# Kernel tuning notes

Hardware: AMD Instinct MI355X
Metric: run time of the kernel (lower is better)

## Reference

```python
import jax, jax.numpy as jnp
import numpy as np

NEG_BIG = -1e38

def setup_inputs() -> dict:
    key = jax.random.key(0)
    kq, kk, kv, kwq, kwk = jax.random.split(key, 5)
    B, S, d_model, d_k, d_v = 4, 4096, 256, 64, 64
    return {
        "q": jax.random.normal(kq, (B, S, d_model), dtype=jnp.float32),
        "k": jax.random.normal(kk, (B, S, d_model), dtype=jnp.float32),
        "v": jax.random.normal(kv, (B, S, d_v), dtype=jnp.float32),
        "w_q": jax.random.normal(kwq, (d_k, d_model), dtype=jnp.float32) * 0.01,
        "w_k": jax.random.normal(kwk, (d_k, d_model), dtype=jnp.float32) * 0.01,
    }

def reference(q, k, v, w_q, w_k):
    d_k = w_q.shape[0]
    temperature = jnp.asarray(np.power(d_k, 0.5), dtype=q.dtype)
    # relu-projected Q, K: [B,S,d_k]
    qp = jax.nn.relu(jnp.einsum("bsm,km->bsk", q, w_q))
    kp = jax.nn.relu(jnp.einsum("bsm,km->bsk", k, w_k))
    # scores [B,S,S]
    attn = jnp.einsum("bqd,bkd->bqk", qp, kp) / temperature
    # force column 0 to -1e38 (inline custom mask)
    attn = attn.at[:, :, 0].set(NEG_BIG)
    attn = jax.nn.softmax(attn, axis=2)
    # dropout is identity in eval / p=0
    out = jnp.einsum("bqk,bkd->bqd", attn, v)
    return out
```

## Files before the change

### kernel.cpp

```cpp
#include <hip/hip_runtime.h>

#define B_    4
#define S_    4096
#define DM    256
#define DK    64
#define NROWS (B_ * S_)
#define LOG2E 1.4426950408889634f
#define PACK_BIAS 0.0028151295f

typedef __attribute__((ext_vector_type(8))) short bfrag;
typedef __attribute__((ext_vector_type(4))) float ffrag;

__device__ __forceinline__ unsigned bf16_rne_hi(float x) {
    unsigned u = __float_as_uint(x);
    return u + 0x7fffu + ((u >> 16) & 1u);
}
__device__ __forceinline__ unsigned short f2bf(float x) {
    return (unsigned short)(bf16_rne_hi(x) >> 16);
}
__device__ __forceinline__ unsigned pack_bf16x2(float lo, float hi) {
    return (bf16_rne_hi(hi) & 0xffff0000u) | (bf16_rne_hi(lo) >> 16);
}

__device__ __forceinline__ float fast_exp2(float x) {
#if __has_builtin(__builtin_amdgcn_exp2f)
    return __builtin_amdgcn_exp2f(x);
#else
    float r;
    asm("v_exp_f32 %0, %1\n\ts_nop 1" : "=v"(r) : "v"(x));
    return r;
#endif
}

__device__ __forceinline__ unsigned trunc_pack_bf16x2(float lo, float hi) {
    return __builtin_amdgcn_perm(__float_as_uint(hi), __float_as_uint(lo),
                                 0x07060302u);
}

__device__ __forceinline__ void proj_step(
    const float4 xv0, const float4 xv1, const unsigned short* wlds,
    int kf, int m, int quad, ffrag acc[4])
{
    union { bfrag v; unsigned u[4]; } pk;
    pk.u[0] = pack_bf16x2(xv0.x, xv0.y);
    pk.u[1] = pack_bf16x2(xv0.z, xv0.w);
    pk.u[2] = pack_bf16x2(xv1.x, xv1.y);
    pk.u[3] = pack_bf16x2(xv1.z, xv1.w);
#pragma unroll
    for (int dt = 0; dt < 4; ++dt) {
        const bfrag Bf = *(const bfrag*)&wlds[(dt * 16 + m) * 264 + kf * 32 + quad * 8];
        acc[dt] = __builtin_amdgcn_mfma_f32_16x16x32_bf16(pk.v, Bf, acc[dt], 0, 0, 0);
    }
}

__global__ __launch_bounds__(256) void fused_prep(
    const float* __restrict__ q, const float* __restrict__ k,
    const float* __restrict__ v, const float* __restrict__ wq,
    const float* __restrict__ wk, unsigned short* __restrict__ vT,
    unsigned short* __restrict__ qpb, unsigned short* __restrict__ kpb)
{
    __shared__ __align__(16) char smem[64 * 264 * 2];
    const int blk  = blockIdx.x;
    const int tid  = threadIdx.x;
    const int lane = tid & 63, w = tid >> 6;

    if (blk < 256) {
        float (*tile)[65] = (float(*)[65])smem;
        const int b = blk >> 6, s0 = (blk & 63) * 64;
#pragma unroll
        for (int i = 0; i < 16; ++i) {
            const int sl = i * 4 + w;
            tile[sl][lane] = v[(b * S_ + s0 + sl) * DK + lane];
        }
        __syncthreads();
        const int t32 = lane >> 5, pos = lane & 31;
        const int keyl = t32 * 32 + ((pos & 1) ? (pos >> 1) + 16 : (pos >> 1));
#pragma unroll
        for (int i = 0; i < 16; ++i) {
            const int d = i * 4 + w;
            vT[((size_t)(b * 128 + (s0 >> 5) + t32) * 64 + d) * 32 + pos] =
                f2bf(tile[keyl][d]);
        }
    } else {
        unsigned short* wlds = (unsigned short*)smem;
        const int pb = blk - 256;
        const int half = pb >> 8, rblk = pb & 255;
        const float* x;
        const float* wsrc;
        unsigned short* o;
        float scale;
        if (half == 0) { x = q; wsrc = wq; o = qpb; scale = 0.125f * LOG2E; }
        else           { x = k; wsrc = wk; o = kpb; scale = 1.0f; }

        const int m = lane & 15, quad = lane >> 4;
        const int rows0 = rblk * 64 + w * 16;
        const float* xrow = x + (size_t)(rows0 + m) * DM + quad * 8;
        const float4* xf4 = (const float4*)xrow;

        float4 xA[4][2];
#pragma unroll
        for (int t = 0; t < 4; ++t) {
            xA[t][0] = xf4[t * 8];
            xA[t][1] = xf4[t * 8 + 1];
        }

#pragma unroll
        for (int i = 0; i < 16; ++i) {
            const int idx4 = i * 256 + tid;
            const int r = idx4 >> 6, c4 = idx4 & 63;
            const float4 wv = ((const float4*)wsrc)[idx4];
            uint2 pk;
            pk.x = pack_bf16x2(wv.x, wv.y);
            pk.y = pack_bf16x2(wv.z, wv.w);
            *(uint2*)&wlds[r * 264 + c4 * 4] = pk;
        }
        __syncthreads();

        ffrag acc[4];
#pragma unroll
        for (int dt = 0; dt < 4; ++dt) acc[dt] = (ffrag)(0.0f);

        float4 xB[4][2];
#pragma unroll
        for (int kf = 0; kf < 4; ++kf) {
            xB[kf][0] = xf4[(kf + 4) * 8];
            xB[kf][1] = xf4[(kf + 4) * 8 + 1];
            proj_step(xA[kf][0], xA[kf][1], wlds, kf, m, quad, acc);
        }
#pragma unroll
        for (int kf = 0; kf < 4; ++kf)
            proj_step(xB[kf][0], xB[kf][1], wlds, kf + 4, m, quad, acc);

#pragma unroll
        for (int dt = 0; dt < 4; ++dt)
#pragma unroll
            for (int r = 0; r < 4; ++r)
                o[(rows0 + quad * 4 + r) * DK + dt * 16 + m] =
                    f2bf(fmaxf(acc[dt][r], 0.0f) * scale);
    }
}

__global__ __launch_bounds__(256) void attn_mfma(
    const unsigned short* __restrict__ qp, const unsigned short* __restrict__ kp,
    const unsigned short* __restrict__ vT, float* __restrict__ out)
{
    __shared__ __align__(16) char smem[20480];
    unsigned short* Plds = (unsigned short*)smem;
    float* red0 = (float*)smem;
    float* red1 = (float*)smem + 2560;

    const int lane = threadIdx.x & 63, w = threadIdx.x >> 6;
    const int m = lane & 15, quad = lane >> 4;

    const int flat = blockIdx.x;
    const int qg   = ((flat & 7) << 6) | (flat >> 3);

    const int qbase = qg * 32;
    const int b = qg >> 7;
    const int kstart = w * 1024;

    bfrag qa[2][2];
#pragma unroll
    for (int mt = 0; mt < 2; ++mt)
#pragma unroll
        for (int kf = 0; kf < 2; ++kf)
            qa[mt][kf] = *(const bfrag*)&qp[(qbase + mt * 16 + m) * DK + kf * 32 + quad * 8];

    ffrag oacc[2][4];
    float dacc[2][4];
#pragma unroll
    for (int mt = 0; mt < 2; ++mt) {
#pragma unroll
        for (int dt = 0; dt < 4; ++dt) oacc[mt][dt] = (ffrag)(0.0f);
#pragma unroll
        for (int r = 0; r < 4; ++r) dacc[mt][r] = 0.0f;
    }

    const unsigned short* kptr = kp + ((size_t)b * S_ + kstart + m) * DK + quad * 8;
    const unsigned short* vptr = vT + ((size_t)(b * 128 + (kstart >> 5)) * 64 + m) * 32 + quad * 8;
    unsigned short* Pw = Plds + w * 1280;

    const ffrag cbias = (ffrag)(PACK_BIAS);

    bfrag kbuf[2][2][2], vbuf[2][4];
#pragma unroll
    for (int kt = 0; kt < 2; ++kt)
#pragma unroll
        for (int kf = 0; kf < 2; ++kf)
            kbuf[0][kt][kf] = *(const bfrag*)(kptr + kt * 1024 + kf * 32);
#pragma unroll
    for (int dt = 0; dt < 4; ++dt)
        vbuf[0][dt] = *(const bfrag*)(vptr + dt * 512);

    bfrag pa0, pa1;

#pragma unroll 2
    for (int jj = 0; jj < 32; ++jj) {
        const int p = jj & 1;

        if (jj < 31) {
            const unsigned short* kn = kptr + (jj + 1) * 2048;
#pragma unroll
            for (int kt = 0; kt < 2; ++kt)
#pragma unroll
                for (int kf = 0; kf < 2; ++kf)
                    kbuf[p ^ 1][kt][kf] = *(const bfrag*)(kn + kt * 1024 + kf * 32);
        }

        if (jj > 0) {
#pragma unroll
            for (int dt = 0; dt < 4; ++dt) {
                oacc[0][dt] = __builtin_amdgcn_mfma_f32_16x16x32_bf16(pa0, vbuf[p ^ 1][dt], oacc[0][dt], 0, 0, 0);
                oacc[1][dt] = __builtin_amdgcn_mfma_f32_16x16x32_bf16(pa1, vbuf[p ^ 1][dt], oacc[1][dt], 0, 0, 0);
            }
        }

        if (jj < 31) {
            const unsigned short* vn = vptr + (jj + 1) * 2048;
#pragma unroll
            for (int dt = 0; dt < 4; ++dt)
                vbuf[p ^ 1][dt] = *(const bfrag*)(vn + dt * 512);
        }

        ffrag s[2][2];
#pragma unroll
        for (int mt = 0; mt < 2; ++mt)
#pragma unroll
            for (int kt = 0; kt < 2; ++kt) {
                ffrag t = __builtin_amdgcn_mfma_f32_16x16x32_bf16(qa[mt][0], kbuf[p][kt][0], cbias, 0, 0, 0);
                s[mt][kt] = __builtin_amdgcn_mfma_f32_16x16x32_bf16(qa[mt][1], kbuf[p][kt][1], t, 0, 0, 0);
            }

        const bool mask0 = (jj == 0) && (w == 0) && (m == 0);
#pragma unroll
        for (int mt = 0; mt < 2; ++mt)
#pragma unroll
            for (int r = 0; r < 4; ++r) {
                float e0 = fast_exp2(s[mt][0][r]);
                float e1 = fast_exp2(s[mt][1][r]);
                if (mask0) e0 = 0.0f;
                dacc[mt][r] += e0 + e1;
                *(unsigned*)&Pw[(mt * 16 + quad * 4 + r) * 40 + m * 2] =
                    trunc_pack_bf16x2(e0, e1);
            }

        pa0 = *(const bfrag*)&Pw[(m) * 40 + quad * 8];
        pa1 = *(const bfrag*)&Pw[(16 + m) * 40 + quad * 8];
    }
#pragma unroll
    for (int dt = 0; dt < 4; ++dt) {
        oacc[0][dt] = __builtin_amdgcn_mfma_f32_16x16x32_bf16(pa0, vbuf[1][dt], oacc[0][dt], 0, 0, 0);
        oacc[1][dt] = __builtin_amdgcn_mfma_f32_16x16x32_bf16(pa1, vbuf[1][dt], oacc[1][dt], 0, 0, 0);
    }

#pragma unroll
    for (int mt = 0; mt < 2; ++mt)
#pragma unroll
        for (int r = 0; r < 4; ++r) {
            float d = dacc[mt][r];
            d += __shfl_xor(d, 1, 64);
            d += __shfl_xor(d, 2, 64);
            d += __shfl_xor(d, 4, 64);
            d += __shfl_xor(d, 8, 64);
            dacc[mt][r] = d;
        }

    __syncthreads();
    if (w >= 2) {
        float* dst = (w == 2) ? red0 : red1;
#pragma unroll
        for (int mt = 0; mt < 2; ++mt) {
#pragma unroll
            for (int dt = 0; dt < 4; ++dt)
#pragma unroll
                for (int r = 0; r < 4; ++r)
                    dst[((mt * 4 + dt) * 4 + r) * 64 + lane] = oacc[mt][dt][r];
#pragma unroll
            for (int r = 0; r < 4; ++r)
                dst[2048 + (mt * 4 + r) * 64 + lane] = dacc[mt][r];
        }
    }
    __syncthreads();
    if (w < 2) {
        const float* src = (w == 0) ? red0 : red1;
#pragma unroll
        for (int mt = 0; mt < 2; ++mt) {
#pragma unroll
            for (int dt = 0; dt < 4; ++dt)
#pragma unroll
                for (int r = 0; r < 4; ++r)
                    oacc[mt][dt][r] += src[((mt * 4 + dt) * 4 + r) * 64 + lane];
#pragma unroll
            for (int r = 0; r < 4; ++r)
                dacc[mt][r] += src[2048 + (mt * 4 + r) * 64 + lane];
        }
    }
    __syncthreads();
    if (w == 1) {
#pragma unroll
        for (int mt = 0; mt < 2; ++mt) {
#pragma unroll
            for (int dt = 0; dt < 4; ++dt)
#pragma unroll
                for (int r = 0; r < 4; ++r)
                    red0[((mt * 4 + dt) * 4 + r) * 64 + lane] = oacc[mt][dt][r];
#pragma unroll
            for (int r = 0; r < 4; ++r)
                red0[2048 + (mt * 4 + r) * 64 + lane] = dacc[mt][r];
        }
    }
    __syncthreads();
    if (w == 0) {
#pragma unroll
        for (int mt = 0; mt < 2; ++mt) {
            float invd[4];
#pragma unroll
            for (int r = 0; r < 4; ++r) {
                const float dv = dacc[mt][r] + red0[2048 + (mt * 4 + r) * 64 + lane];
                invd[r] = 1.0f / dv;
            }
#pragma unroll
            for (int dt = 0; dt < 4; ++dt)
#pragma unroll
                for (int r = 0; r < 4; ++r) {
                    const float nv = oacc[mt][dt][r] + red0[((mt * 4 + dt) * 4 + r) * 64 + lane];
                    out[(size_t)(qbase + mt * 16 + quad * 4 + r) * DK + dt * 16 + m] =
                        nv * invd[r];
                }
        }
    }
}

extern "C" void kernel_launch(void* const* d_in, const int* in_sizes, int n_in,
                              void* d_out, int out_size, void* d_ws, size_t ws_size,
                              hipStream_t stream)
{
    const float* q  = (const float*)d_in[0];
    const float* k  = (const float*)d_in[1];
    const float* v  = (const float*)d_in[2];
    const float* wq = (const float*)d_in[3];
    const float* wk = (const float*)d_in[4];
    float* out = (float*)d_out;

    char* p = (char*)d_ws;
    unsigned short* qpb = (unsigned short*)p;   p += (size_t)NROWS * DK * 2;
    unsigned short* kpb = (unsigned short*)p;   p += (size_t)NROWS * DK * 2;
    unsigned short* vT  = (unsigned short*)p;

    fused_prep<<<768, 256, 0, stream>>>(q, k, v, wq, wk, vT, qpb, kpb);
    attn_mfma<<<512, 256, 0, stream>>>(qpb, kpb, vT, out);
}
```

Measured before the change: 133.0 us.

## Enlarge attention block to 64 query rows with 8 waves splitting keys

Each block of the attention kernel now handles 64 query rows instead of 32, using 8 wavefronts that each cover 512 keys, so every K/V fragment loaded is reused across four 16-row tiles instead of two. The grid drops to 256 blocks of 512 threads, with a deeper shared-memory tree reduction across the 8 waves done in two halves. This halves the global K/V traffic per query row. In exchange it raises register pressure (launch bounds 512,2), allows fewer blocks than CUs to fill the device, and adds more barriers in the final reduction.

```diff
diff --git a/kernel.cpp b/kernel.cpp
--- a/kernel.cpp
+++ b/kernel.cpp
@@ -140,36 +140,35 @@
     }
 }
 
-__global__ __launch_bounds__(256) void attn_mfma(
+__global__ __launch_bounds__(512, 2) void attn_mfma(
     const unsigned short* __restrict__ qp, const unsigned short* __restrict__ kp,
     const unsigned short* __restrict__ vT, float* __restrict__ out)
 {
-    __shared__ __align__(16) char smem[20480];
+    __shared__ __align__(16) char smem[40960];
     unsigned short* Plds = (unsigned short*)smem;
-    float* red0 = (float*)smem;
-    float* red1 = (float*)smem + 2560;
-
-    const int lane = threadIdx.x & 63, w = threadIdx.x >> 6;
+
+    const int tid  = threadIdx.x;
+    const int lane = tid & 63, w = tid >> 6;
     const int m = lane & 15, quad = lane >> 4;
 
     const int flat = blockIdx.x;
-    const int qg   = ((flat & 7) << 6) | (flat >> 3);
-
-    const int qbase = qg * 32;
-    const int b = qg >> 7;
-    const int kstart = w * 1024;
-
-    bfrag qa[2][2];
-#pragma unroll
-    for (int mt = 0; mt < 2; ++mt)
+    const int qg   = ((flat & 7) << 5) | (flat >> 3);
+
+    const int qbase = qg * 64;
+    const int b = qg >> 6;
+    const int kstart = w * 512;
+
+    bfrag qa[4][2];
+#pragma unroll
+    for (int mt = 0; mt < 4; ++mt)
 #pragma unroll
         for (int kf = 0; kf < 2; ++kf)
             qa[mt][kf] = *(const bfrag*)&qp[(qbase + mt * 16 + m) * DK + kf * 32 + quad * 8];
 
-    ffrag oacc[2][4];
-    float dacc[2][4];
-#pragma unroll
-    for (int mt = 0; mt < 2; ++mt) {
+    ffrag oacc[4][4];
+    float dacc[4][4];
+#pragma unroll
+    for (int mt = 0; mt < 4; ++mt) {
 #pragma unroll
         for (int dt = 0; dt < 4; ++dt) oacc[mt][dt] = (ffrag)(0.0f);
 #pragma unroll
@@ -178,7 +177,7 @@
 
     const unsigned short* kptr = kp + ((size_t)b * S_ + kstart + m) * DK + quad * 8;
     const unsigned short* vptr = vT + ((size_t)(b * 128 + (kstart >> 5)) * 64 + m) * 32 + quad * 8;
-    unsigned short* Pw = Plds + w * 1280;
+    unsigned short* Pw = Plds + w * 2560;
 
     const ffrag cbias = (ffrag)(PACK_BIAS);
 
@@ -192,13 +191,13 @@
     for (int dt = 0; dt < 4; ++dt)
         vbuf[0][dt] = *(const bfrag*)(vptr + dt * 512);
 
-    bfrag pa0, pa1;
+    bfrag pa0, pa1, pa2, pa3;
 
 #pragma unroll 2
-    for (int jj = 0; jj < 32; ++jj) {
+    for (int jj = 0; jj < 16; ++jj) {
         const int p = jj & 1;
 
-        if (jj < 31) {
+        if (jj < 15) {
             const unsigned short* kn = kptr + (jj + 1) * 2048;
 #pragma unroll
             for (int kt = 0; kt < 2; ++kt)
@@ -212,49 +211,78 @@
             for (int dt = 0; dt < 4; ++dt) {
                 oacc[0][dt] = __builtin_amdgcn_mfma_f32_16x16x32_bf16(pa0, vbuf[p ^ 1][dt], oacc[0][dt], 0, 0, 0);
                 oacc[1][dt] = __builtin_amdgcn_mfma_f32_16x16x32_bf16(pa1, vbuf[p ^ 1][dt], oacc[1][dt], 0, 0, 0);
-            }
-        }
-
-        if (jj < 31) {
+                oacc[2][dt] = __builtin_amdgcn_mfma_f32_16x16x32_bf16(pa2, vbuf[p ^ 1][dt], oacc[2][dt], 0, 0, 0);
+                oacc[3][dt] = __builtin_amdgcn_mfma_f32_16x16x32_bf16(pa3, vbuf[p ^ 1][dt], oacc[3][dt], 0, 0, 0);
+            }
+        }
+
+        if (jj < 15) {
             const unsigned short* vn = vptr + (jj + 1) * 2048;
 #pragma unroll
             for (int dt = 0; dt < 4; ++dt)
                 vbuf[p ^ 1][dt] = *(const bfrag*)(vn + dt * 512);
         }
 
-        ffrag s[2][2];
-#pragma unroll
-        for (int mt = 0; mt < 2; ++mt)
-#pragma unroll
-            for (int kt = 0; kt < 2; ++kt) {
-                ffrag t = __builtin_amdgcn_mfma_f32_16x16x32_bf16(qa[mt][0], kbuf[p][kt][0], cbias, 0, 0, 0);
-                s[mt][kt] = __builtin_amdgcn_mfma_f32_16x16x32_bf16(qa[mt][1], kbuf[p][kt][1], t, 0, 0, 0);
-            }
-
         const bool mask0 = (jj == 0) && (w == 0) && (m == 0);
-#pragma unroll
-        for (int mt = 0; mt < 2; ++mt)
-#pragma unroll
-            for (int r = 0; r < 4; ++r) {
-                float e0 = fast_exp2(s[mt][0][r]);
-                float e1 = fast_exp2(s[mt][1][r]);
-                if (mask0) e0 = 0.0f;
-                dacc[mt][r] += e0 + e1;
-                *(unsigned*)&Pw[(mt * 16 + quad * 4 + r) * 40 + m * 2] =
-                    trunc_pack_bf16x2(e0, e1);
-            }
+
+        {
+            ffrag s[2][2];
+#pragma unroll
+            for (int mt = 0; mt < 2; ++mt)
+#pragma unroll
+                for (int kt = 0; kt < 2; ++kt) {
+                    ffrag t = __builtin_amdgcn_mfma_f32_16x16x32_bf16(qa[mt][0], kbuf[p][kt][0], cbias, 0, 0, 0);
+                    s[mt][kt] = __builtin_amdgcn_mfma_f32_16x16x32_bf16(qa[mt][1], kbuf[p][kt][1], t, 0, 0, 0);
+                }
+#pragma unroll
+            for (int mt = 0; mt < 2; ++mt)
+#pragma unroll
+                for (int r = 0; r < 4; ++r) {
+                    float e0 = fast_exp2(s[mt][0][r]);
+                    float e1 = fast_exp2(s[mt][1][r]);
+                    if (mask0) e0 = 0.0f;
+                    dacc[mt][r] += e0 + e1;
+                    *(unsigned*)&Pw[(mt * 16 + quad * 4 + r) * 40 + m * 2] =
+                        trunc_pack_bf16x2(e0, e1);
+                }
+        }
+        {
+            ffrag s[2][2];
+#pragma unroll
+            for (int mt = 2; mt < 4; ++mt)
+#pragma unroll
+                for (int kt = 0; kt < 2; ++kt) {
+                    ffrag t = __builtin_amdgcn_mfma_f32_16x16x32_bf16(qa[mt][0], kbuf[p][kt][0], cbias, 0, 0, 0);
+                    s[mt - 2][kt] = __builtin_amdgcn_mfma_f32_16x16x32_bf16(qa[mt][1], kbuf[p][kt][1], t, 0, 0, 0);
+                }
+#pragma unroll
+            for (int mt = 2; mt < 4; ++mt)
+#pragma unroll
+                for (int r = 0; r < 4; ++r) {
+                    float e0 = fast_exp2(s[mt - 2][0][r]);
+                    float e1 = fast_exp2(s[mt - 2][1][r]);
+                    if (mask0) e0 = 0.0f;
+                    dacc[mt][r] += e0 + e1;
+                    *(unsigned*)&Pw[(mt * 16 + quad * 4 + r) * 40 + m * 2] =
+                        trunc_pack_bf16x2(e0, e1);
+                }
+        }
 
         pa0 = *(const bfrag*)&Pw[(m) * 40 + quad * 8];
         pa1 = *(const bfrag*)&Pw[(16 + m) * 40 + quad * 8];
+        pa2 = *(const bfrag*)&Pw[(32 + m) * 40 + quad * 8];
+        pa3 = *(const bfrag*)&Pw[(48 + m) * 40 + quad * 8];
     }
 #pragma unroll
     for (int dt = 0; dt < 4; ++dt) {
         oacc[0][dt] = __builtin_amdgcn_mfma_f32_16x16x32_bf16(pa0, vbuf[1][dt], oacc[0][dt], 0, 0, 0);
         oacc[1][dt] = __builtin_amdgcn_mfma_f32_16x16x32_bf16(pa1, vbuf[1][dt], oacc[1][dt], 0, 0, 0);
-    }
-
-#pragma unroll
-    for (int mt = 0; mt < 2; ++mt)
+        oacc[2][dt] = __builtin_amdgcn_mfma_f32_16x16x32_bf16(pa2, vbuf[1][dt], oacc[2][dt], 0, 0, 0);
+        oacc[3][dt] = __builtin_amdgcn_mfma_f32_16x16x32_bf16(pa3, vbuf[1][dt], oacc[3][dt], 0, 0, 0);
+    }
+
+#pragma unroll
+    for (int mt = 0; mt < 4; ++mt)
 #pragma unroll
         for (int r = 0; r < 4; ++r) {
             float d = dacc[mt][r];
@@ -265,68 +293,104 @@
             dacc[mt][r] = d;
         }
 
-    __syncthreads();
-    if (w >= 2) {
-        float* dst = (w == 2) ? red0 : red1;
-#pragma unroll
-        for (int mt = 0; mt < 2; ++mt) {
-#pragma unroll
-            for (int dt = 0; dt < 4; ++dt)
+    float* red = (float*)smem;
+#pragma unroll
+    for (int half = 0; half < 2; ++half) {
+        const int mt0 = half * 2;
+        __syncthreads();
+        if (w >= 4) {
+            float* dst = red + (w - 4) * 2560;
+#pragma unroll
+            for (int mr = 0; mr < 2; ++mr) {
+#pragma unroll
+                for (int dt = 0; dt < 4; ++dt)
+#pragma unroll
+                    for (int r = 0; r < 4; ++r)
+                        dst[((mr * 4 + dt) * 4 + r) * 64 + lane] = oacc[mt0 + mr][dt][r];
 #pragma unroll
                 for (int r = 0; r < 4; ++r)
-                    dst[((mt * 4 + dt) * 4 + r) * 64 + lane] = oacc[mt][dt][r];
-#pragma unroll
-            for (int r = 0; r < 4; ++r)
-                dst[2048 + (mt * 4 + r) * 64 + lane] = dacc[mt][r];
-        }
-    }
-    __syncthreads();
-    if (w < 2) {
-        const float* src = (w == 0) ? red0 : red1;
-#pragma unroll
-        for (int mt = 0; mt < 2; ++mt) {
-#pragma unroll
-            for (int dt = 0; dt < 4; ++dt)
+                    dst[2048 + (mr * 4 + r) * 64 + lane] = dacc[mt0 + mr][r];
+            }
+        }
+        __syncthreads();
+        if (w < 4) {
+            const float* src = red + w * 2560;
+#pragma unroll
+            for (int mr = 0; mr < 2; ++mr) {
+#pragma unroll
+                for (int dt = 0; dt < 4; ++dt)
+#pragma unroll
+                    for (int r = 0; r < 4; ++r)
+                        oacc[mt0 + mr][dt][r] += src[((mr * 4 + dt) * 4 + r) * 64 + lane];
 #pragma unroll
                 for (int r = 0; r < 4; ++r)
-                    oacc[mt][dt][r] += src[((mt * 4 + dt) * 4 + r) * 64 + lane];
-#pragma unroll
-            for (int r = 0; r < 4; ++r)
-                dacc[mt][r] += src[2048 + (mt * 4 + r) * 64 + lane];
-        }
-    }
-    __syncthreads();
-    if (w == 1) {
-#pragma unroll
-        for (int mt = 0; mt < 2; ++mt) {
-#pragma unroll
-            for (int dt = 0; dt < 4; ++dt)
+                    dacc[mt0 + mr][r] += src[2048 + (mr * 4 + r) * 64 + lane];
+            }
+        }
+        __syncthreads();
+        if (w >= 2 && w < 4) {
+            float* dst = red + (w - 2) * 2560;
+#pragma unroll
+            for (int mr = 0; mr < 2; ++mr) {
+#pragma unroll
+                for (int dt = 0; dt < 4; ++dt)
+#pragma unroll
+                    for (int r = 0; r < 4; ++r)
+                        dst[((mr * 4 + dt) * 4 + r) * 64 + lane] = oacc[mt0 + mr][dt][r];
 #pragma unroll
                 for (int r = 0; r < 4; ++r)
-                    red0[((mt * 4 + dt) * 4 + r) * 64 + lane] = oacc[mt][dt][r];
-#pragma unroll
-            for (int r = 0; r < 4; ++r)
-                red0[2048 + (mt * 4 + r) * 64 + lane] = dacc[mt][r];
-        }
-    }
-    __syncthreads();
-    if (w == 0) {
-#pragma unroll
-        for (int mt = 0; mt < 2; ++mt) {
-            float invd[4];
-#pragma unroll
-            for (int r = 0; r < 4; ++r) {
-                const float dv = dacc[mt][r] + red0[2048 + (mt * 4 + r) * 64 + lane];
-                invd[r] = 1.0f / dv;
-            }
-#pragma unroll
-            for (int dt = 0; dt < 4; ++dt)
+                    dst[2048 + (mr * 4 + r) * 64 + lane] = dacc[mt0 + mr][r];
+            }
+        }
+        __syncthreads();
+        if (w < 2) {
+            const float* src = red + w * 2560;
+#pragma unroll
+            for (int mr = 0; mr < 2; ++mr) {
+#pragma unroll
+                for (int dt = 0; dt < 4; ++dt)
+#pragma unroll
+                    for (int r = 0; r < 4; ++r)
+                        oacc[mt0 + mr][dt][r] += src[((mr * 4 + dt) * 4 + r) * 64 + lane];
+#pragma unroll
+                for (int r = 0; r < 4; ++r)
+                    dacc[mt0 + mr][r] += src[2048 + (mr * 4 + r) * 64 + lane];
+            }
+        }
+        __syncthreads();
+        if (w == 1) {
+#pragma unroll
+            for (int mr = 0; mr < 2; ++mr) {
+#pragma unroll
+                for (int dt = 0; dt < 4; ++dt)
+#pragma unroll
+                    for (int r = 0; r < 4; ++r)
+                        red[((mr * 4 + dt) * 4 + r) * 64 + lane] = oacc[mt0 + mr][dt][r];
+#pragma unroll
+                for (int r = 0; r < 4; ++r)
+                    red[2048 + (mr * 4 + r) * 64 + lane] = dacc[mt0 + mr][r];
+            }
+        }
+        __syncthreads();
+        if (w == 0) {
+#pragma unroll
+            for (int mr = 0; mr < 2; ++mr) {
+                const int mt = mt0 + mr;
+                float invd[4];
 #pragma unroll
                 for (int r = 0; r < 4; ++r) {
-                    const float nv = oacc[mt][dt][r] + red0[((mt * 4 + dt) * 4 + r) * 64 + lane];
-                    out[(size_t)(qbase + mt * 16 + quad * 4 + r) * DK + dt * 16 + m] =
-                        nv * invd[r];
+                    const float dv = dacc[mt][r] + red[2048 + (mr * 4 + r) * 64 + lane];
+                    invd[r] = 1.0f / dv;
                 }
+#pragma unroll
+                for (int dt = 0; dt < 4; ++dt)
+#pragma unroll
+                    for (int r = 0; r < 4; ++r) {
+                        const float nv = oacc[mt][dt][r] + red[((mr * 4 + dt) * 4 + r) * 64 + lane];
+                        out[(size_t)(qbase + mt * 16 + quad * 4 + r) * DK + dt * 16 + m] =
+                            nv * invd[r];
+                    }
+            }
         }
     }
 }
@@ -348,5 +412,5 @@
     unsigned short* vT  = (unsigned short*)p;
 
     fused_prep<<<768, 256, 0, stream>>>(q, k, v, wq, wk, vT, qpb, kpb);
-    attn_mfma<<<512, 256, 0, stream>>>(qpb, kpb, vT, out);
-}
+    attn_mfma<<<256, 512, 0, stream>>>(qpb, kpb, vT, out);
+}
```

Measured after the change: 115.0 us. -13.5%, faster.
